# Kernel tuning notes

Measured on AMD Instinct MI355X. Metric: run time of the kernel, lower is better.

The kernel has to match this reference:

```python
import jax, jax.numpy as jnp
import numpy as np

D_K = 64
D_MODEL = 1024
SEQ = 4096
BATCH = 4


def setup_inputs() -> dict:
    key = jax.random.key(0)
    ks = jax.random.split(key, 7)
    s = 1.0 / np.sqrt(D_MODEL)
    return {
        "x": jax.random.normal(ks[0], (BATCH, SEQ, D_MODEL), dtype=jnp.float32),
        "wq": jax.random.uniform(ks[1], (D_K, D_MODEL), jnp.float32, -s, s),
        "bq": jax.random.uniform(ks[2], (D_K,), jnp.float32, -s, s),
        "wk": jax.random.uniform(ks[3], (D_K, D_MODEL), jnp.float32, -s, s),
        "bk": jax.random.uniform(ks[4], (D_K,), jnp.float32, -s, s),
        "wv": jax.random.uniform(ks[5], (D_K, D_MODEL), jnp.float32, -s, s),
        "bv": jax.random.uniform(ks[6], (D_K,), jnp.float32, -s, s),
    }


def reference(x, wq, bq, wk, bk, wv, bv):
    # q,k,v: [B,T,d_k]
    q = jnp.einsum('btc,dc->btd', x, wq) + bq
    k = jnp.einsum('btc,dc->btd', x, wk) + bk
    v = jnp.einsum('btc,dc->btd', x, wv) + bv
    scale = 1.0 / np.sqrt(D_K).astype(np.float32)
    scores = jnp.einsum('bqd,bkd->bqk', q, k) * scale  # [B,T,T]
    T = x.shape[1]
    causal = jnp.tril(jnp.ones((T, T), dtype=bool))
    scores = jnp.where(causal, scores, -jnp.inf)
    sm = jax.nn.softmax(scores, axis=-1)
    return jnp.einsum('bqk,bkd->bqd', sm, v)
```

## Files before the change

kernel.cpp:

```cpp
#include <hip/hip_runtime.h>

typedef __attribute__((ext_vector_type(8))) short short8;
typedef __attribute__((ext_vector_type(4))) float f32x4;

#define D_KV   64
#define SEQ    4096
#define NBATCH 4
#define DMODEL 1024

static __device__ __forceinline__ unsigned short f32_to_bf16(float f) {
  unsigned u = __builtin_bit_cast(unsigned, f);
  u = (u + 0x7FFFu + ((u >> 16) & 1u)) >> 16;
  return (unsigned short)u;
}

__global__ __launch_bounds__(256) void xfrag_kernel(
    const float* __restrict__ x, unsigned short* __restrict__ xfrag) {
  __shared__ unsigned short lt[16 * 1024];
  const int tid = threadIdx.x;
  const long T = blockIdx.x;
  {
    const int row = tid >> 4, seg = tid & 15;
    const float* src = x + (T * 16 + row) * DMODEL + seg * 64;
    unsigned short* dst = lt + row * 1024 + seg * 64;
#pragma unroll
    for (int j = 0; j < 8; ++j) {
      const f32x4 f0 = *reinterpret_cast<const f32x4*>(src + j * 8);
      const f32x4 f1 = *reinterpret_cast<const f32x4*>(src + j * 8 + 4);
      short8 s;
#pragma unroll
      for (int q = 0; q < 4; ++q) {
        s[q] = (short)f32_to_bf16(f0[q]);
        s[4 + q] = (short)f32_to_bf16(f1[q]);
      }
      *reinterpret_cast<short8*>(dst + j * 8) = s;
    }
  }
  __syncthreads();
  unsigned short* dst = xfrag + T * 16384;
#pragma unroll
  for (int i = 0; i < 8; ++i) {
    const int slot = i * 256 + tid;
    const int lane2 = slot & 63, ks = slot >> 6;
    const short8 v = *reinterpret_cast<const short8*>(
        lt + (lane2 & 15) * 1024 + ks * 32 + (lane2 >> 4) * 8);
    *reinterpret_cast<short8*>(dst + slot * 8) = v;
  }
}

__global__ __launch_bounds__(256) void wcvt_kernel(
    const float* __restrict__ wq, const float* __restrict__ wk,
    const float* __restrict__ wv, unsigned short* __restrict__ wfrag) {
  const int fid = blockIdx.x * 256 + threadIdx.x;
  const int nt = fid >> 11, ks = (fid >> 6) & 31, lane = fid & 63;
  const int l16 = lane & 15, lq = lane >> 4;
  const float* w = (nt < 4) ? wq : (nt < 8) ? wk : wv;
  const float* src = w + ((nt & 3) * 16 + l16) * DMODEL + ks * 32 + lq * 8;
  short8 v;
#pragma unroll
  for (int j = 0; j < 8; ++j) v[j] = (short)f32_to_bf16(src[j]);
  *reinterpret_cast<short8*>(wfrag + (long)fid * 8) = v;
}

__global__ __launch_bounds__(512, 1) void qkv_proj_kernel(
    const unsigned short* __restrict__ xfrag,
    const unsigned short* __restrict__ wfrag,
    const float* __restrict__ bq, const float* __restrict__ bk,
    const float* __restrict__ bv,
    unsigned short* __restrict__ Qf, unsigned short* __restrict__ Kf,
    unsigned short* __restrict__ Vf) {
  const int tid = threadIdx.x, lane = tid & 63, wave = tid >> 6;
  const int l16 = lane & 15, lq = lane >> 4;
  const int trio = wave & 3;
  const long T0 = (long)blockIdx.x * 4 + (wave >> 2) * 2;

  const unsigned short* a0 = xfrag + T0 * 16384 + lane * 8;
  const unsigned short* a1 = xfrag + (T0 + 1) * 16384 + lane * 8;
  const unsigned short* wbase = wfrag + (long)(3 * trio) * 16384 + lane * 8;

  f32x4 acc[3][2];
#pragma unroll
  for (int i = 0; i < 3; ++i)
#pragma unroll
    for (int p = 0; p < 2; ++p) acc[i][p] = (f32x4){0.f, 0.f, 0.f, 0.f};

#pragma unroll
  for (int ck = 0; ck < 8; ++ck) {
    short8 a[4][2], bw[12];
#pragma unroll
    for (int kc = 0; kc < 4; ++kc) {
      a[kc][0] = *reinterpret_cast<const short8*>(a0 + (ck * 4 + kc) * 512);
      a[kc][1] = *reinterpret_cast<const short8*>(a1 + (ck * 4 + kc) * 512);
    }
#pragma unroll
    for (int j = 0; j < 12; ++j)
      bw[j] = *reinterpret_cast<const short8*>(
          wbase + (long)(j >> 2) * 16384 + (ck * 4 + (j & 3)) * 512);
#pragma unroll
    for (int kc = 0; kc < 4; ++kc)
#pragma unroll
      for (int i = 0; i < 3; ++i) {
        acc[i][0] = __builtin_amdgcn_mfma_f32_16x16x32_bf16(
            a[kc][0], bw[i * 4 + kc], acc[i][0], 0, 0, 0);
        acc[i][1] = __builtin_amdgcn_mfma_f32_16x16x32_bf16(
            a[kc][1], bw[i * 4 + kc], acc[i][1], 0, 0, 0);
      }
  }

#pragma unroll
  for (int i = 0; i < 3; ++i) {
    const int nt = 3 * trio + i;
    const int mat = nt >> 2;
    const int dcol = ((nt & 3) << 4) | l16;
    const float bias = (mat == 0 ? bq : mat == 1 ? bk : bv)[dcol];
    const int c = dcol >> 5, lqp = (dcol >> 3) & 3, jj = dcol & 7;
#pragma unroll
    for (int p = 0; p < 2; ++p)
#pragma unroll
      for (int rr = 0; rr < 4; ++rr) {
        const long t = (T0 + p) * 16 + lq * 4 + rr;
        const float sum = acc[i][p][rr] + bias;
        if (mat == 0) {
          Qf[(((t >> 4) * 2 + c) * 64 + lqp * 16 + (t & 15)) * 8 + jj] =
              f32_to_bf16(sum * 0.125f);
        } else if (mat == 1) {
          Kf[((((t >> 6) * 4 + ((t >> 4) & 3)) * 2 + c) * 64 + lqp * 16 +
              (t & 15)) * 8 + jj] = f32_to_bf16(sum);
        } else {
          Vf[((((t >> 6) * 4 + (dcol >> 4)) * 2 + ((t >> 5) & 1)) * 64 +
              ((t >> 3) & 3) * 16 + (dcol & 15)) * 8 + (t & 7)] =
              f32_to_bf16(sum);
        }
      }
  }
}

__global__ __launch_bounds__(512) void attn_kernel(
    const unsigned short* __restrict__ Qf, const unsigned short* __restrict__ Kf,
    const unsigned short* __restrict__ Vf, float* __restrict__ out) {
  __shared__ __align__(16) unsigned short p_lds[8][16][72];
  __shared__ __align__(16) float lds_o[8][16][68];
  __shared__ float lds_ml[8][16][2];
  __shared__ float lds_gl[16];

  const int tid = threadIdx.x;
  const int lane = tid & 63;
  const int wave = tid >> 6;
  const int l16 = lane & 15, lq = lane >> 4;
  const int b = blockIdx.y;
  const int tile = 255 - blockIdx.x;
  const int qbase = tile * 16;
  const long qrow = (long)b * SEQ + qbase;

  short8 qf[2];
#pragma unroll
  for (int c = 0; c < 2; ++c)
    qf[c] = *reinterpret_cast<const short8*>(
        Qf + ((qrow >> 4) * 2 + c) * 512 + lane * 8);

  f32x4 o[4];
#pragma unroll
  for (int dt = 0; dt < 4; ++dt) o[dt] = (f32x4){0.f, 0.f, 0.f, 0.f};
  float m = -INFINITY, ell = 0.f;

  const long ktile0 = (long)b * 64;
  const int nkv = qbase / 64 + 1;
  for (int kt = wave; kt < nkv; kt += 8) {
    const int kvbase = kt * 64;
    const unsigned short* kb = Kf + (ktile0 + kt) * 4096 + lane * 8;
    const unsigned short* vb = Vf + (ktile0 + kt) * 4096 + lane * 8;
    f32x4 s[4];
#pragma unroll
    for (int ct = 0; ct < 4; ++ct) s[ct] = (f32x4){0.f, 0.f, 0.f, 0.f};
#pragma unroll
    for (int ct = 0; ct < 4; ++ct)
#pragma unroll
      for (int c = 0; c < 2; ++c) {
        short8 kf = *reinterpret_cast<const short8*>(kb + (ct * 2 + c) * 512);
        s[ct] = __builtin_amdgcn_mfma_f32_16x16x32_bf16(kf, qf[c], s[ct], 0, 0, 0);
      }
    if (kt == nkv - 1) {
      const int qg = qbase + l16;
#pragma unroll
      for (int ct = 0; ct < 4; ++ct)
#pragma unroll
        for (int r = 0; r < 4; ++r)
          if (kvbase + ct * 16 + lq * 4 + r > qg) s[ct][r] = -INFINITY;
    }
    float mx = -INFINITY;
#pragma unroll
    for (int ct = 0; ct < 4; ++ct)
#pragma unroll
      for (int r = 0; r < 4; ++r) mx = fmaxf(mx, s[ct][r]);
    mx = fmaxf(mx, __shfl_xor(mx, 16, 64));
    mx = fmaxf(mx, __shfl_xor(mx, 32, 64));
    const float nm = fmaxf(m, mx);
    const float alpha = __expf(m - nm);
    float rs = 0.f;
#pragma unroll
    for (int ct = 0; ct < 4; ++ct)
#pragma unroll
      for (int r = 0; r < 4; ++r) {
        const float p = __expf(s[ct][r] - nm);
        s[ct][r] = p;
        rs += p;
      }
    rs += __shfl_xor(rs, 16, 64);
    rs += __shfl_xor(rs, 32, 64);
    ell = ell * alpha + rs;
    m = nm;
#pragma unroll
    for (int dt = 0; dt < 4; ++dt) o[dt] *= alpha;
#pragma unroll
    for (int ct = 0; ct < 4; ++ct)
#pragma unroll
      for (int r = 0; r < 4; ++r)
        p_lds[wave][l16][ct * 16 + lq * 4 + r] = f32_to_bf16(s[ct][r]);
    short8 pf[2];
#pragma unroll
    for (int c = 0; c < 2; ++c)
      pf[c] = *reinterpret_cast<const short8*>(&p_lds[wave][l16][c * 32 + lq * 8]);
#pragma unroll
    for (int dt = 0; dt < 4; ++dt)
#pragma unroll
      for (int c = 0; c < 2; ++c) {
        short8 vf = *reinterpret_cast<const short8*>(vb + (dt * 2 + c) * 512);
        o[dt] = __builtin_amdgcn_mfma_f32_16x16x32_bf16(vf, pf[c], o[dt], 0, 0, 0);
      }
  }

  if (lane < 16) {
    lds_ml[wave][l16][0] = m;
    lds_ml[wave][l16][1] = ell;
  }
  __syncthreads();
  float g = -INFINITY;
#pragma unroll
  for (int w2 = 0; w2 < 8; ++w2) g = fmaxf(g, lds_ml[w2][l16][0]);
  float gl = 0.f;
#pragma unroll
  for (int w2 = 0; w2 < 8; ++w2)
    gl += lds_ml[w2][l16][1] * __expf(lds_ml[w2][l16][0] - g);
  const float myscale = __expf(m - g);
  if (wave == 0 && lane < 16) lds_gl[l16] = gl;
#pragma unroll
  for (int dt = 0; dt < 4; ++dt)
#pragma unroll
    for (int r = 0; r < 4; ++r)
      lds_o[wave][l16][dt * 16 + lq * 4 + r] = o[dt][r] * myscale;
  __syncthreads();
#pragma unroll
  for (int j = 0; j < 2; ++j) {
    const int e = tid + 512 * j;
    const int row = e >> 6, col = e & 63;
    float sum = 0.f;
#pragma unroll
    for (int w2 = 0; w2 < 8; ++w2) sum += lds_o[w2][row][col];
    out[(qrow + row) * D_KV + col] = sum / lds_gl[row];
  }
}

extern "C" void kernel_launch(void* const* d_in, const int* in_sizes, int n_in,
                              void* d_out, int out_size, void* d_ws, size_t ws_size,
                              hipStream_t stream) {
  const float* x  = (const float*)d_in[0];
  const float* wq = (const float*)d_in[1];
  const float* bq = (const float*)d_in[2];
  const float* wk = (const float*)d_in[3];
  const float* bk = (const float*)d_in[4];
  const float* wv = (const float*)d_in[5];
  const float* bv = (const float*)d_in[6];
  float* out = (float*)d_out;

  unsigned short* ws    = (unsigned short*)d_ws;
  unsigned short* wfrag = ws;
  unsigned short* Qf    = ws + 196608;
  unsigned short* Kf    = Qf + 1048576;
  unsigned short* Vf    = Kf + 1048576;
  unsigned short* xfrag = Vf + 1048576;

  xfrag_kernel<<<1024, 256, 0, stream>>>(x, xfrag);
  wcvt_kernel<<<96, 256, 0, stream>>>(wq, wk, wv, wfrag);
  qkv_proj_kernel<<<256, 512, 0, stream>>>(xfrag, wfrag, bq, bk, bv, Qf, Kf, Vf);
  dim3 ag(256, NBATCH);
  attn_kernel<<<ag, 512, 0, stream>>>(Qf, Kf, Vf, out);
}
```

Measured before the change: 72.43 us.

## Stage projection weights in LDS and split QKV output columns across blocks

The QKV projection kernel now assigns each block one quarter of the output columns (three 16-wide tiles) and 16 token tiles. Each block copies its 96 KB weight slice into LDS once using direct global-to-LDS loads, and every wave then reads its B fragments from LDS instead of global memory. This cuts repeated global and L2 traffic for the weights. In exchange, each wave now reads the x fragments for its own token tiles, so activation reads happen four times across the quarters. The large LDS footprint limits how many blocks fit per CU, and the launch_bounds min-blocks hint was removed.

```diff
diff --git a/kernel.cpp b/kernel.cpp
--- a/kernel.cpp
+++ b/kernel.cpp
@@ -12,6 +12,12 @@
   unsigned u = __builtin_bit_cast(unsigned, f);
   u = (u + 0x7FFFu + ((u >> 16) & 1u)) >> 16;
   return (unsigned short)u;
+}
+
+static __device__ __forceinline__ void gload_lds16(const void* gsrc, void* ldst) {
+  __builtin_amdgcn_global_load_lds(
+      (const __attribute__((address_space(1))) void*)gsrc,
+      (__attribute__((address_space(3))) void*)ldst, 16, 0, 0);
 }
 
 __global__ __launch_bounds__(256) void xfrag_kernel(
@@ -62,21 +68,33 @@
   *reinterpret_cast<short8*>(wfrag + (long)fid * 8) = v;
 }
 
-__global__ __launch_bounds__(512, 1) void qkv_proj_kernel(
+__global__ __launch_bounds__(512) void qkv_proj_kernel(
     const unsigned short* __restrict__ xfrag,
     const unsigned short* __restrict__ wfrag,
     const float* __restrict__ bq, const float* __restrict__ bk,
     const float* __restrict__ bv,
     unsigned short* __restrict__ Qf, unsigned short* __restrict__ Kf,
     unsigned short* __restrict__ Vf) {
+  __shared__ __align__(16) unsigned short lds_w[49152];
   const int tid = threadIdx.x, lane = tid & 63, wave = tid >> 6;
   const int l16 = lane & 15, lq = lane >> 4;
-  const int trio = wave & 3;
-  const long T0 = (long)blockIdx.x * 4 + (wave >> 2) * 2;
-
+  const int quarter = blockIdx.x & 3;
+  const long group = blockIdx.x >> 2;
+
+  const unsigned char* wsrc =
+      (const unsigned char*)(wfrag + (long)(3 * quarter) * 16384);
+  unsigned char* wl = (unsigned char*)lds_w;
+#pragma unroll
+  for (int s = 0; s < 12; ++s) {
+    const int slot = wave * 12 + s;
+    gload_lds16(wsrc + slot * 1024 + lane * 16, wl + slot * 1024);
+  }
+  __syncthreads();
+
+  const long T0 = group * 16 + 2 * wave;
   const unsigned short* a0 = xfrag + T0 * 16384 + lane * 8;
-  const unsigned short* a1 = xfrag + (T0 + 1) * 16384 + lane * 8;
-  const unsigned short* wbase = wfrag + (long)(3 * trio) * 16384 + lane * 8;
+  const unsigned short* a1 = a0 + 16384;
+  const unsigned char* wlane = wl + lane * 16;
 
   f32x4 acc[3][2];
 #pragma unroll
@@ -93,9 +111,11 @@
       a[kc][1] = *reinterpret_cast<const short8*>(a1 + (ck * 4 + kc) * 512);
     }
 #pragma unroll
-    for (int j = 0; j < 12; ++j)
-      bw[j] = *reinterpret_cast<const short8*>(
-          wbase + (long)(j >> 2) * 16384 + (ck * 4 + (j & 3)) * 512);
+    for (int i = 0; i < 3; ++i)
+#pragma unroll
+      for (int kc = 0; kc < 4; ++kc)
+        bw[i * 4 + kc] = *reinterpret_cast<const short8*>(
+            wlane + (i * 32 + ck * 4 + kc) * 1024);
 #pragma unroll
     for (int kc = 0; kc < 4; ++kc)
 #pragma unroll
@@ -109,7 +129,7 @@
 
 #pragma unroll
   for (int i = 0; i < 3; ++i) {
-    const int nt = 3 * trio + i;
+    const int nt = 3 * quarter + i;
     const int mat = nt >> 2;
     const int dcol = ((nt & 3) << 4) | l16;
     const float bias = (mat == 0 ? bq : mat == 1 ? bk : bv)[dcol];
```

Result: slower. 77.39 us (+6.9%).
